# Performance work log

Measured on AMD Instinct MI355X. Metric: run time of the kernel, lower is better.

## Reference

```python
import jax, jax.numpy as jnp
import numpy as np

B, S, H, DEPTH = 2, 2048, 8, 64
D_MODEL = H * DEPTH  # 512


def setup_inputs() -> dict:
    key = jax.random.key(0)
    ks = jax.random.split(key, 6)
    s = 0.02
    return {
        "emb_x": jax.random.normal(ks[0], (B, S, D_MODEL), dtype=jnp.float32),
        "pe_rel_t": jax.random.normal(ks[1], (B, S, D_MODEL), dtype=jnp.float32),
        "Wq": jax.random.normal(ks[2], (D_MODEL, D_MODEL), dtype=jnp.float32) * s,
        "bq": jnp.zeros((D_MODEL,), dtype=jnp.float32),
        "Wk": jax.random.normal(ks[3], (D_MODEL, D_MODEL), dtype=jnp.float32) * s,
        "bk": jnp.zeros((D_MODEL,), dtype=jnp.float32),
        "Wv": jax.random.normal(ks[4], (D_MODEL, D_MODEL), dtype=jnp.float32) * s,
        "bv": jnp.zeros((D_MODEL,), dtype=jnp.float32),
        "Wo": jax.random.normal(ks[5], (D_MODEL, D_MODEL), dtype=jnp.float32) * s,
        "bo": jnp.zeros((D_MODEL,), dtype=jnp.float32),
    }


def _split_heads(x):
    # [B, S, D_MODEL] -> [B, H, S, DEPTH]
    b, s, _ = x.shape
    return x.reshape(b, s, H, DEPTH).transpose(0, 2, 1, 3)


def reference(emb_x, pe_rel_t, Wq, bq, Wk, bk, Wv, bv, Wo, bo):
    # RPE attention: content and relative-position streams share WQ/WK.
    Q_c = _split_heads(emb_x @ Wq + bq)
    Q_r = _split_heads(pe_rel_t @ Wq + bq)
    K_c = _split_heads(emb_x @ Wk + bk)
    K_r = _split_heads(pe_rel_t @ Wk + bk)
    V_c = _split_heads(emb_x @ Wv + bv)

    logits = (
        jnp.einsum("bhqd,bhkd->bhqk", Q_c, K_c)
        + jnp.einsum("bhqd,bhkd->bhqk", Q_r, K_c)
        + jnp.einsum("bhqd,bhkd->bhqk", Q_c, K_r)
    ) / jnp.sqrt(jnp.asarray(DEPTH, dtype=emb_x.dtype))

    attn = jax.nn.softmax(logits, axis=-1)  # [B, H, S, S]
    z = jnp.einsum("bhqk,bhkd->bhqd", attn, V_c)  # [B, H, S, DEPTH]
    z = z.transpose(0, 2, 1, 3).reshape(emb_x.shape[0], -1, D_MODEL)
    out = z @ Wo + bo
    return out, attn
```

## Files before the change

### kernel.cpp

```cpp
#include <hip/hip_runtime.h>
#include <hip/hip_bf16.h>


typedef __bf16 bf16;
typedef bf16 bf16x4 __attribute__((ext_vector_type(4)));
typedef bf16 bf16x8 __attribute__((ext_vector_type(8)));
typedef float f32x4 __attribute__((ext_vector_type(4)));

#define B_ 2
#define S_ 2048
#define H_ 8
#define D_ 64
#define DM_ 512
#define M_ 4096

__global__ __launch_bounds__(256) void pack_x(const float4* __restrict__ emb,
                                              const float4* __restrict__ pe,
                                              bf16* __restrict__ xb,
                                              bf16* __restrict__ xp,
                                              bf16* __restrict__ xs) {
    int i = blockIdx.x * 256 + threadIdx.x;
    float4 a = emb[i], b = pe[i];
    int o = i * 4;
    bf16x4 va, vp, vs;
    va.x = (bf16)a.x; va.y = (bf16)a.y; va.z = (bf16)a.z; va.w = (bf16)a.w;
    vp.x = (bf16)b.x; vp.y = (bf16)b.y; vp.z = (bf16)b.z; vp.w = (bf16)b.w;
    vs.x = (bf16)(a.x + b.x); vs.y = (bf16)(a.y + b.y);
    vs.z = (bf16)(a.z + b.z); vs.w = (bf16)(a.w + b.w);
    *(bf16x4*)(xb + o) = va;
    *(bf16x4*)(xp + o) = vp;
    *(bf16x4*)(xs + o) = vs;
}

__global__ __launch_bounds__(256) void pack_w4(const float* __restrict__ Wq,
                                               const float* __restrict__ Wk,
                                               const float* __restrict__ Wv,
                                               const float* __restrict__ Wo,
                                               bf16* __restrict__ WT) {
    __shared__ float t[32][33];
    const float* W = (blockIdx.z == 0) ? Wq : (blockIdx.z == 1) ? Wk
                   : (blockIdx.z == 2) ? Wv : Wo;
    bf16* dst = WT + (long)blockIdx.z * (DM_ * DM_);
    const int r = threadIdx.x >> 5, c = threadIdx.x & 31;
    const int kb = blockIdx.x * 32, nb = blockIdx.y * 32;
    for (int i = 0; i < 4; ++i)
        t[r + 8 * i][c] = W[(long)(kb + r + 8 * i) * 512 + nb + c];
    __syncthreads();
    for (int i = 0; i < 4; ++i)
        dst[(long)(nb + r + 8 * i) * 512 + kb + c] = (bf16)t[c][r + 8 * i];
}

__global__ __launch_bounds__(256) void proj_fused(
    const bf16* __restrict__ Xb, const bf16* __restrict__ Xp,
    const bf16* __restrict__ Xs, const bf16* __restrict__ WT,
    const float* __restrict__ bq, const float* __restrict__ bk,
    const float* __restrict__ bv,
    bf16* __restrict__ Qc, bf16* __restrict__ Qr, bf16* __restrict__ Kc,
    bf16* __restrict__ Ks, bf16* __restrict__ Vt) {
    __shared__ bf16 As[64][72];
    __shared__ bf16 Bs[64][72];

    const int z = blockIdx.z;
    const bf16* A = (z == 1) ? Xp : (z == 3) ? Xs : Xb;
    const bf16* BT = WT + (long)(z >> 1) * (DM_ * DM_);
    const float* bias = (z >= 4) ? bv : (z >= 2) ? bk : bq;
    const float bscale = (z == 3) ? 2.f : 1.f;
    bf16* dst = (z == 0) ? Qc : (z == 1) ? Qr : (z == 2) ? Kc
              : (z == 3) ? Ks : Vt;
    const bool vmode = (z == 4);

    const int tid = threadIdx.x;
    const int lane = tid & 63;
    const int wave = tid >> 6;
    const int wm = wave >> 1, wn = wave & 1;
    const int row0 = blockIdx.x * 64;
    const int col0 = blockIdx.y * 64;
    const int lm = lane & 15, lk = (lane >> 4) * 8;
    const int r0 = tid >> 3, sg0 = (tid & 7) * 8;

    f32x4 acc[2][2] = {{{0.f,0.f,0.f,0.f},{0.f,0.f,0.f,0.f}},
                       {{0.f,0.f,0.f,0.f},{0.f,0.f,0.f,0.f}}};

    bf16x8 ra[2], rb[2];
    auto load_ab = [&](int k0) {
        ra[0] = *(const bf16x8*)(A + (long)(row0 + r0) * 512 + k0 + sg0);
        ra[1] = *(const bf16x8*)(A + (long)(row0 + r0 + 32) * 512 + k0 + sg0);
        rb[0] = *(const bf16x8*)(BT + (long)(col0 + r0) * 512 + k0 + sg0);
        rb[1] = *(const bf16x8*)(BT + (long)(col0 + r0 + 32) * 512 + k0 + sg0);
    };

    load_ab(0);
    for (int k0 = 0; k0 < 512; k0 += 64) {
        *(bf16x8*)&As[r0][sg0]      = ra[0];
        *(bf16x8*)&As[r0 + 32][sg0] = ra[1];
        *(bf16x8*)&Bs[r0][sg0]      = rb[0];
        *(bf16x8*)&Bs[r0 + 32][sg0] = rb[1];
        __syncthreads();
        if (k0 < 448) load_ab(k0 + 64);
        for (int kk = 0; kk < 64; kk += 32) {
            bf16x8 af[2], bfr[2];
            for (int t = 0; t < 2; ++t) {
                af[t]  = *(const bf16x8*)&As[wm * 32 + t * 16 + lm][kk + lk];
                bfr[t] = *(const bf16x8*)&Bs[wn * 32 + t * 16 + lm][kk + lk];
            }
            for (int mt = 0; mt < 2; ++mt)
                for (int nt = 0; nt < 2; ++nt)
                    acc[mt][nt] = __builtin_amdgcn_mfma_f32_16x16x32_bf16(
                        af[mt], bfr[nt], acc[mt][nt], 0, 0, 0);
        }
        __syncthreads();
    }

    const int rbase = (lane >> 4) * 4;
    for (int mt = 0; mt < 2; ++mt)
        for (int nt = 0; nt < 2; ++nt)
            for (int r = 0; r < 4; ++r) {
                int row = row0 + wm * 32 + mt * 16 + rbase + r;
                int col = col0 + wn * 32 + nt * 16 + lm;
                float v = acc[mt][nt][r] + bias[col] * bscale;
                int b = row >> 11, s = row & 2047, h = col >> 6, d = col & 63;
                if (!vmode)
                    dst[(((long)(b * H_ + h) * S_ + s) * 64) + d] = (bf16)v;
                else
                    dst[(((long)(b * H_ + h) * 64 + d) * S_) + s] = (bf16)v;
            }
}

__global__ __launch_bounds__(256) void proj_out(const bf16* __restrict__ Zb,
                                                const bf16* __restrict__ WoT,
                                                const float* __restrict__ bo,
                                                float* __restrict__ Out) {
    __shared__ bf16 As[64][72];
    __shared__ bf16 Bs[64][72];
    const int tid = threadIdx.x;
    const int lane = tid & 63;
    const int wave = tid >> 6;
    const int wm = wave >> 1, wn = wave & 1;
    const int row0 = blockIdx.x * 64;
    const int col0 = blockIdx.y * 64;
    const int lm = lane & 15, lk = (lane >> 4) * 8;
    const int r0 = tid >> 3, sg0 = (tid & 7) * 8;

    f32x4 acc[2][2] = {{{0.f,0.f,0.f,0.f},{0.f,0.f,0.f,0.f}},
                       {{0.f,0.f,0.f,0.f},{0.f,0.f,0.f,0.f}}};

    bf16x8 ra[2], rb[2];
    auto load_ab = [&](int k0) {
        const int acol = k0 + sg0;
        const int h = acol >> 6, d = acol & 63;
        {
            int arow = row0 + r0;
            int b = arow >> 11, s = arow & 2047;
            ra[0] = *(const bf16x8*)(Zb + (((long)(b * H_ + h) * S_ + s) * 64) + d);
        }
        {
            int arow = row0 + r0 + 32;
            int b = arow >> 11, s = arow & 2047;
            ra[1] = *(const bf16x8*)(Zb + (((long)(b * H_ + h) * S_ + s) * 64) + d);
        }
        rb[0] = *(const bf16x8*)(WoT + (long)(col0 + r0) * 512 + k0 + sg0);
        rb[1] = *(const bf16x8*)(WoT + (long)(col0 + r0 + 32) * 512 + k0 + sg0);
    };

    load_ab(0);
    for (int k0 = 0; k0 < 512; k0 += 64) {
        *(bf16x8*)&As[r0][sg0]      = ra[0];
        *(bf16x8*)&As[r0 + 32][sg0] = ra[1];
        *(bf16x8*)&Bs[r0][sg0]      = rb[0];
        *(bf16x8*)&Bs[r0 + 32][sg0] = rb[1];
        __syncthreads();
        if (k0 < 448) load_ab(k0 + 64);
        for (int kk = 0; kk < 64; kk += 32) {
            bf16x8 af[2], bfr[2];
            for (int t = 0; t < 2; ++t) {
                af[t]  = *(const bf16x8*)&As[wm * 32 + t * 16 + lm][kk + lk];
                bfr[t] = *(const bf16x8*)&Bs[wn * 32 + t * 16 + lm][kk + lk];
            }
            for (int mt = 0; mt < 2; ++mt)
                for (int nt = 0; nt < 2; ++nt)
                    acc[mt][nt] = __builtin_amdgcn_mfma_f32_16x16x32_bf16(
                        af[mt], bfr[nt], acc[mt][nt], 0, 0, 0);
        }
        __syncthreads();
    }

    const int rbase = (lane >> 4) * 4;
    for (int mt = 0; mt < 2; ++mt)
        for (int nt = 0; nt < 2; ++nt)
            for (int r = 0; r < 4; ++r) {
                int row = row0 + wm * 32 + mt * 16 + rbase + r;
                int col = col0 + wn * 32 + nt * 16 + lm;
                Out[(long)row * 512 + col] = acc[mt][nt][r] + bo[col];
            }
}

__global__ __launch_bounds__(512, 4) void attn_fwd(const bf16* __restrict__ Qc,
                                                   const bf16* __restrict__ Qr,
                                                   const bf16* __restrict__ Kc,
                                                   const bf16* __restrict__ Ks,
                                                   const bf16* __restrict__ Vt,
                                                   bf16* __restrict__ Zb,
                                                   float* __restrict__ invR) {
    __shared__ bf16 Kcs[2][64][72];
    __shared__ bf16 Kss[2][64][72];
    __shared__ bf16 Vts[2][64][72];
    __shared__ bf16 ptile[8][16][40];
    __shared__ float rsLds[4][16];

    const int tid = threadIdx.x, lane = tid & 63, wave = tid >> 6;
    const int grp = wave >> 2, w4 = wave & 3;
    const int bh = blockIdx.x >> 5;
    const int qt = blockIdx.x & 31;
    const int qw = qt * 64 + w4 * 16;
    const long kbase = (long)bh * (S_ * 64);
    const long vbase = (long)bh * (64 * S_);
    const int lm = lane & 15, lk = (lane >> 4) * 8;
    const int gtid = tid & 255;
    const int r0 = gtid >> 3, sg0 = (gtid & 7) * 8;
    const float SC = 0.125f;

    bf16x8 qcf[2], qrf[2];
    for (int kt = 0; kt < 2; ++kt) {
        long off = kbase + (long)(qw + lm) * 64 + kt * 32 + lk;
        qcf[kt] = *(const bf16x8*)(Qc + off);
        qrf[kt] = *(const bf16x8*)(Qr + off);
    }

    float rsum[4] = {0.f, 0.f, 0.f, 0.f};
    f32x4 zacc[4] = {{0.f,0.f,0.f,0.f},{0.f,0.f,0.f,0.f},
                     {0.f,0.f,0.f,0.f},{0.f,0.f,0.f,0.f}};

    bf16x8 rk[2], rs[2], rv[2];
    auto load_kv = [&](int key0) {
        rk[0] = *(const bf16x8*)(Kc + kbase + (long)(key0 + r0) * 64 + sg0);
        rk[1] = *(const bf16x8*)(Kc + kbase + (long)(key0 + r0 + 32) * 64 + sg0);
        rs[0] = *(const bf16x8*)(Ks + kbase + (long)(key0 + r0) * 64 + sg0);
        rs[1] = *(const bf16x8*)(Ks + kbase + (long)(key0 + r0 + 32) * 64 + sg0);
        rv[0] = *(const bf16x8*)(Vt + vbase + (long)r0 * S_ + key0 + sg0);
        rv[1] = *(const bf16x8*)(Vt + vbase + (long)(r0 + 32) * S_ + key0 + sg0);
    };

    load_kv(grp * 64);
    for (int t = grp; t < 32; t += 2) {
        __syncthreads();
        *(bf16x8*)&Kcs[grp][r0][sg0]      = rk[0];
        *(bf16x8*)&Kcs[grp][r0 + 32][sg0] = rk[1];
        *(bf16x8*)&Kss[grp][r0][sg0]      = rs[0];
        *(bf16x8*)&Kss[grp][r0 + 32][sg0] = rs[1];
        *(bf16x8*)&Vts[grp][r0][sg0]      = rv[0];
        *(bf16x8*)&Vts[grp][r0 + 32][sg0] = rv[1];
        __syncthreads();
        if (t + 2 < 32) load_kv((t + 2) * 64);

        for (int pair = 0; pair < 2; ++pair) {
            for (int nt = 0; nt < 2; ++nt) {
                const int keyl = pair * 32 + nt * 16;
                f32x4 acc = {0.f, 0.f, 0.f, 0.f};
                for (int kt = 0; kt < 2; ++kt) {
                    bf16x8 bs = *(const bf16x8*)&Kss[grp][keyl + lm][kt * 32 + lk];
                    bf16x8 bc = *(const bf16x8*)&Kcs[grp][keyl + lm][kt * 32 + lk];
                    acc = __builtin_amdgcn_mfma_f32_16x16x32_bf16(qcf[kt], bs, acc, 0, 0, 0);
                    acc = __builtin_amdgcn_mfma_f32_16x16x32_bf16(qrf[kt], bc, acc, 0, 0, 0);
                }
                for (int r = 0; r < 4; ++r) {
                    float p = __expf(acc[r] * SC);
                    rsum[r] += p;
                    ptile[wave][(lane >> 4) * 4 + r][nt * 16 + lm] = (bf16)p;
                }
            }
            bf16x8 pa = *(const bf16x8*)&ptile[wave][lm][lk];
            for (int nt = 0; nt < 4; ++nt) {
                bf16x8 vb = *(const bf16x8*)&Vts[grp][nt * 16 + lm][pair * 32 + lk];
                zacc[nt] = __builtin_amdgcn_mfma_f32_16x16x32_bf16(pa, vb, zacc[nt], 0, 0, 0);
            }
        }
    }

    for (int r = 0; r < 4; ++r) {
        float s = rsum[r];
        s += __shfl_xor(s, 1);
        s += __shfl_xor(s, 2);
        s += __shfl_xor(s, 4);
        s += __shfl_xor(s, 8);
        rsum[r] = s;
    }

    __syncthreads();
    float* zp = (float*)&Kcs[0][0][0];
    const int qlb = (lane >> 4) * 4;
    if (grp == 1) {
        for (int nt = 0; nt < 4; ++nt)
            for (int r = 0; r < 4; ++r)
                zp[(w4 * 16 + qlb + r) * 68 + nt * 16 + lm] = zacc[nt][r];
        if (lm == 0)
            for (int r = 0; r < 4; ++r) rsLds[w4][qlb + r] = rsum[r];
    }
    __syncthreads();
    if (grp == 0) {
        float inv_r[4];
        for (int r = 0; r < 4; ++r)
            inv_r[r] = 1.0f / (rsum[r] + rsLds[w4][qlb + r]);
        for (int nt = 0; nt < 4; ++nt)
            for (int r = 0; r < 4; ++r) {
                float zv = zacc[nt][r] + zp[(w4 * 16 + qlb + r) * 68 + nt * 16 + lm];
                Zb[kbase + (long)(qw + qlb + r) * 64 + nt * 16 + lm] =
                    (bf16)(zv * inv_r[r]);
            }
        if (lm == 0)
            for (int r = 0; r < 4; ++r)
                invR[bh * S_ + qw + qlb + r] = inv_r[r];
    }
}

__global__ __launch_bounds__(256) void attn_wr(const bf16* __restrict__ Qc,
                                               const bf16* __restrict__ Qr,
                                               const bf16* __restrict__ Kc,
                                               const bf16* __restrict__ Ks,
                                               const float* __restrict__ invR,
                                               float* __restrict__ attn_out) {
    __shared__ bf16 Kcs[64][72];
    __shared__ bf16 Kss[64][72];

    const int tid = threadIdx.x, lane = tid & 63, wave = tid >> 6;
    const int bh = blockIdx.z;
    const int qt = blockIdx.x;
    const int kc = blockIdx.y;
    const int qw = qt * 64 + wave * 16;
    const long kbase = (long)bh * (S_ * 64);
    const long abase = (long)bh * S_ * S_;
    const int lm = lane & 15, lk = (lane >> 4) * 8;
    const int kg = lane >> 4;
    const int r0 = tid >> 3, sg0 = (tid & 7) * 8;
    const float SC = 0.125f;

    bf16x8 qcf[2], qrf[2];
    for (int kt = 0; kt < 2; ++kt) {
        long off = kbase + (long)(qw + lm) * 64 + kt * 32 + lk;
        qcf[kt] = *(const bf16x8*)(Qc + off);
        qrf[kt] = *(const bf16x8*)(Qr + off);
    }
    const float invq = invR[bh * S_ + qw + lm];
    const long qrow = abase + (long)(qw + lm) * S_;

    bf16x8 rk[2], rs[2];
    auto load_k = [&](int key0) {
        rk[0] = *(const bf16x8*)(Kc + kbase + (long)(key0 + r0) * 64 + sg0);
        rk[1] = *(const bf16x8*)(Kc + kbase + (long)(key0 + r0 + 32) * 64 + sg0);
        rs[0] = *(const bf16x8*)(Ks + kbase + (long)(key0 + r0) * 64 + sg0);
        rs[1] = *(const bf16x8*)(Ks + kbase + (long)(key0 + r0 + 32) * 64 + sg0);
    };

    load_k(kc * 512);
    for (int t = 0; t < 8; ++t) {
        const int key0 = kc * 512 + t * 64;
        __syncthreads();
        *(bf16x8*)&Kcs[r0][sg0]      = rk[0];
        *(bf16x8*)&Kcs[r0 + 32][sg0] = rk[1];
        *(bf16x8*)&Kss[r0][sg0]      = rs[0];
        *(bf16x8*)&Kss[r0 + 32][sg0] = rs[1];
        __syncthreads();
        if (t < 7) load_k(key0 + 64);

        for (int nt = 0; nt < 4; ++nt) {
            const int keyl = nt * 16;
            f32x4 acc = {0.f, 0.f, 0.f, 0.f};
            for (int kt = 0; kt < 2; ++kt) {
                bf16x8 bs = *(const bf16x8*)&Kss[keyl + lm][kt * 32 + lk];
                bf16x8 bc = *(const bf16x8*)&Kcs[keyl + lm][kt * 32 + lk];
                acc = __builtin_amdgcn_mfma_f32_16x16x32_bf16(bs, qcf[kt], acc, 0, 0, 0);
                acc = __builtin_amdgcn_mfma_f32_16x16x32_bf16(bc, qrf[kt], acc, 0, 0, 0);
            }
            f32x4 p;
            for (int r = 0; r < 4; ++r) p[r] = __expf(acc[r] * SC) * invq;
            f32x4* dst = (f32x4*)(attn_out + qrow + key0 + keyl + kg * 4);
            __builtin_nontemporal_store(p, dst);
        }
    }
}

extern "C" void kernel_launch(void* const* d_in, const int* in_sizes, int n_in,
                              void* d_out, int out_size, void* d_ws, size_t ws_size,
                              hipStream_t stream) {
    const float* emb = (const float*)d_in[0];
    const float* pe  = (const float*)d_in[1];
    const float* Wq  = (const float*)d_in[2];
    const float* bq  = (const float*)d_in[3];
    const float* Wk  = (const float*)d_in[4];
    const float* bk  = (const float*)d_in[5];
    const float* Wv  = (const float*)d_in[6];
    const float* bv  = (const float*)d_in[7];
    const float* Wo  = (const float*)d_in[8];
    const float* bo  = (const float*)d_in[9];

    float* outp = (float*)d_out;
    float* attn = outp + (long)B_ * S_ * DM_;

    char* w = (char*)d_ws;
    const long SZ_X = (long)M_ * DM_ * 2;
    const long SZ_W = (long)DM_ * DM_ * 2;
    bf16* Xb  = (bf16*)(w);
    bf16* Xp  = (bf16*)(w + SZ_X);
    bf16* Xs  = (bf16*)(w + 2 * SZ_X);
    bf16* WqT = (bf16*)(w + 3 * SZ_X);
    bf16* WoT = (bf16*)(w + 3 * SZ_X + 3 * SZ_W);
    char* p2  = w + 3 * SZ_X + 4 * SZ_W;
    bf16* Qc  = (bf16*)(p2);
    bf16* Qr  = (bf16*)(p2 + SZ_X);
    bf16* Kc  = (bf16*)(p2 + 2 * SZ_X);
    bf16* Ks  = (bf16*)(p2 + 3 * SZ_X);
    bf16* Vt  = (bf16*)(p2 + 4 * SZ_X);
    bf16* Zb  = (bf16*)(p2 + 5 * SZ_X);
    float* invR = (float*)(p2 + 6 * SZ_X);

    pack_x<<<(M_ * DM_ / 4) / 256, 256, 0, stream>>>(
        (const float4*)emb, (const float4*)pe, Xb, Xp, Xs);
    pack_w4<<<dim3(16, 16, 4), 256, 0, stream>>>(Wq, Wk, Wv, Wo, WqT);

    proj_fused<<<dim3(M_ / 64, DM_ / 64, 5), 256, 0, stream>>>(
        Xb, Xp, Xs, WqT, bq, bk, bv, Qc, Qr, Kc, Ks, Vt);

    attn_fwd<<<B_ * H_ * (S_ / 64), 512, 0, stream>>>(
        Qc, Qr, Kc, Ks, Vt, Zb, invR);

    attn_wr<<<dim3(S_ / 64, 4, B_ * H_), 256, 0, stream>>>(
        Qc, Qr, Kc, Ks, invR, attn);

    proj_out<<<dim3(M_ / 64, DM_ / 64), 256, 0, stream>>>(Zb, WoT, bo, outp);
}
```

Baseline: 427.3 us.

## Fuse attention-probability write pass into forward attention kernel

Merges the separate attn_wr kernel into the forward attention kernel. After computing Z and the row sums, each block recomputes logits for its query tile over half the keys per wave group and writes the normalized probabilities, passing inverse row sums through LDS instead of global memory. It also swizzles the block index so concurrently running blocks spread across heads. This removes a launch, the invR round trip and the reload of Q fragments, but the write phase now runs on 512 blocks instead of the separate kernel's larger grid and inherits the fused kernel's register and occupancy limits.

```diff
diff --git a/kernel.cpp b/kernel.cpp
--- a/kernel.cpp
+++ b/kernel.cpp
@@ -194,27 +194,30 @@
             }
 }
 
-__global__ __launch_bounds__(512, 4) void attn_fwd(const bf16* __restrict__ Qc,
+__global__ __launch_bounds__(512, 4) void attn_all(const bf16* __restrict__ Qc,
                                                    const bf16* __restrict__ Qr,
                                                    const bf16* __restrict__ Kc,
                                                    const bf16* __restrict__ Ks,
                                                    const bf16* __restrict__ Vt,
                                                    bf16* __restrict__ Zb,
-                                                   float* __restrict__ invR) {
+                                                   float* __restrict__ attn_out) {
     __shared__ bf16 Kcs[2][64][72];
     __shared__ bf16 Kss[2][64][72];
     __shared__ bf16 Vts[2][64][72];
     __shared__ bf16 ptile[8][16][40];
     __shared__ float rsLds[4][16];
+    __shared__ float invLds[4][16];
 
     const int tid = threadIdx.x, lane = tid & 63, wave = tid >> 6;
     const int grp = wave >> 2, w4 = wave & 3;
-    const int bh = blockIdx.x >> 5;
-    const int qt = blockIdx.x & 31;
+    const int swz = (blockIdx.x & 7) * 64 + (blockIdx.x >> 3);
+    const int bh = swz >> 5;
+    const int qt = swz & 31;
     const int qw = qt * 64 + w4 * 16;
     const long kbase = (long)bh * (S_ * 64);
     const long vbase = (long)bh * (64 * S_);
     const int lm = lane & 15, lk = (lane >> 4) * 8;
+    const int kg = lane >> 4;
     const int gtid = tid & 255;
     const int r0 = gtid >> 3, sg0 = (gtid & 7) * 8;
     const float SC = 0.125f;
@@ -238,6 +241,12 @@
         rs[1] = *(const bf16x8*)(Ks + kbase + (long)(key0 + r0 + 32) * 64 + sg0);
         rv[0] = *(const bf16x8*)(Vt + vbase + (long)r0 * S_ + key0 + sg0);
         rv[1] = *(const bf16x8*)(Vt + vbase + (long)(r0 + 32) * S_ + key0 + sg0);
+    };
+    auto load_k = [&](int key0) {
+        rk[0] = *(const bf16x8*)(Kc + kbase + (long)(key0 + r0) * 64 + sg0);
+        rk[1] = *(const bf16x8*)(Kc + kbase + (long)(key0 + r0 + 32) * 64 + sg0);
+        rs[0] = *(const bf16x8*)(Ks + kbase + (long)(key0 + r0) * 64 + sg0);
+        rs[1] = *(const bf16x8*)(Ks + kbase + (long)(key0 + r0 + 32) * 64 + sg0);
     };
 
     load_kv(grp * 64);
@@ -276,6 +285,8 @@
         }
     }
 
+    load_k(grp * 1024);
+
     for (int r = 0; r < 4; ++r) {
         float s = rsum[r];
         s += __shfl_xor(s, 1);
@@ -307,66 +318,28 @@
                     (bf16)(zv * inv_r[r]);
             }
         if (lm == 0)
-            for (int r = 0; r < 4; ++r)
-                invR[bh * S_ + qw + qlb + r] = inv_r[r];
-    }
-}
-
-__global__ __launch_bounds__(256) void attn_wr(const bf16* __restrict__ Qc,
-                                               const bf16* __restrict__ Qr,
-                                               const bf16* __restrict__ Kc,
-                                               const bf16* __restrict__ Ks,
-                                               const float* __restrict__ invR,
-                                               float* __restrict__ attn_out) {
-    __shared__ bf16 Kcs[64][72];
-    __shared__ bf16 Kss[64][72];
-
-    const int tid = threadIdx.x, lane = tid & 63, wave = tid >> 6;
-    const int bh = blockIdx.z;
-    const int qt = blockIdx.x;
-    const int kc = blockIdx.y;
-    const int qw = qt * 64 + wave * 16;
-    const long kbase = (long)bh * (S_ * 64);
-    const long abase = (long)bh * S_ * S_;
-    const int lm = lane & 15, lk = (lane >> 4) * 8;
-    const int kg = lane >> 4;
-    const int r0 = tid >> 3, sg0 = (tid & 7) * 8;
-    const float SC = 0.125f;
-
-    bf16x8 qcf[2], qrf[2];
-    for (int kt = 0; kt < 2; ++kt) {
-        long off = kbase + (long)(qw + lm) * 64 + kt * 32 + lk;
-        qcf[kt] = *(const bf16x8*)(Qc + off);
-        qrf[kt] = *(const bf16x8*)(Qr + off);
-    }
-    const float invq = invR[bh * S_ + qw + lm];
-    const long qrow = abase + (long)(qw + lm) * S_;
-
-    bf16x8 rk[2], rs[2];
-    auto load_k = [&](int key0) {
-        rk[0] = *(const bf16x8*)(Kc + kbase + (long)(key0 + r0) * 64 + sg0);
-        rk[1] = *(const bf16x8*)(Kc + kbase + (long)(key0 + r0 + 32) * 64 + sg0);
-        rs[0] = *(const bf16x8*)(Ks + kbase + (long)(key0 + r0) * 64 + sg0);
-        rs[1] = *(const bf16x8*)(Ks + kbase + (long)(key0 + r0 + 32) * 64 + sg0);
-    };
-
-    load_k(kc * 512);
-    for (int t = 0; t < 8; ++t) {
-        const int key0 = kc * 512 + t * 64;
-        __syncthreads();
-        *(bf16x8*)&Kcs[r0][sg0]      = rk[0];
-        *(bf16x8*)&Kcs[r0 + 32][sg0] = rk[1];
-        *(bf16x8*)&Kss[r0][sg0]      = rs[0];
-        *(bf16x8*)&Kss[r0 + 32][sg0] = rs[1];
-        __syncthreads();
-        if (t < 7) load_k(key0 + 64);
+            for (int r = 0; r < 4; ++r) invLds[w4][qlb + r] = inv_r[r];
+    }
+    __syncthreads();
+    const float invq = invLds[w4][lm];
+    const long qrow = (long)bh * S_ * S_ + (long)(qw + lm) * S_;
+
+    for (int t2 = 0; t2 < 16; ++t2) {
+        const int key0 = grp * 1024 + t2 * 64;
+        __syncthreads();
+        *(bf16x8*)&Kcs[grp][r0][sg0]      = rk[0];
+        *(bf16x8*)&Kcs[grp][r0 + 32][sg0] = rk[1];
+        *(bf16x8*)&Kss[grp][r0][sg0]      = rs[0];
+        *(bf16x8*)&Kss[grp][r0 + 32][sg0] = rs[1];
+        __syncthreads();
+        if (t2 < 15) load_k(key0 + 64);
 
         for (int nt = 0; nt < 4; ++nt) {
             const int keyl = nt * 16;
             f32x4 acc = {0.f, 0.f, 0.f, 0.f};
             for (int kt = 0; kt < 2; ++kt) {
-                bf16x8 bs = *(const bf16x8*)&Kss[keyl + lm][kt * 32 + lk];
-                bf16x8 bc = *(const bf16x8*)&Kcs[keyl + lm][kt * 32 + lk];
+                bf16x8 bs = *(const bf16x8*)&Kss[grp][keyl + lm][kt * 32 + lk];
+                bf16x8 bc = *(const bf16x8*)&Kcs[grp][keyl + lm][kt * 32 + lk];
                 acc = __builtin_amdgcn_mfma_f32_16x16x32_bf16(bs, qcf[kt], acc, 0, 0, 0);
                 acc = __builtin_amdgcn_mfma_f32_16x16x32_bf16(bc, qrf[kt], acc, 0, 0, 0);
             }
@@ -410,7 +383,6 @@
     bf16* Ks  = (bf16*)(p2 + 3 * SZ_X);
     bf16* Vt  = (bf16*)(p2 + 4 * SZ_X);
     bf16* Zb  = (bf16*)(p2 + 5 * SZ_X);
-    float* invR = (float*)(p2 + 6 * SZ_X);
 
     pack_x<<<(M_ * DM_ / 4) / 256, 256, 0, stream>>>(
         (const float4*)emb, (const float4*)pe, Xb, Xp, Xs);
@@ -419,11 +391,8 @@
     proj_fused<<<dim3(M_ / 64, DM_ / 64, 5), 256, 0, stream>>>(
         Xb, Xp, Xs, WqT, bq, bk, bv, Qc, Qr, Kc, Ks, Vt);
 
-    attn_fwd<<<B_ * H_ * (S_ / 64), 512, 0, stream>>>(
-        Qc, Qr, Kc, Ks, Vt, Zb, invR);
-
-    attn_wr<<<dim3(S_ / 64, 4, B_ * H_), 256, 0, stream>>>(
-        Qc, Qr, Kc, Ks, invR, attn);
+    attn_all<<<B_ * H_ * (S_ / 64), 512, 0, stream>>>(
+        Qc, Qr, Kc, Ks, Vt, Zb, attn);
 
     proj_out<<<dim3(M_ / 64, DM_ / 64), 256, 0, stream>>>(Zb, WoT, bo, outp);
 }
```

Result: no change. 423.1 us (-1.0%).
